# Kernel tuning notes

Hardware: AMD Instinct MI355X
Metric: run time of the kernel (lower is better)

The kernel has to match this reference:

```python
import jax, jax.numpy as jnp
import numpy as np

N, R, IN_DIM, OUT_DIM, MODE = 16, 128, 64, 64, 16


def setup_inputs() -> dict:
    key = jax.random.key(0)
    k1, k2, k3, k4, k5 = jax.random.split(key, 5)
    # xavier_normal-like scale used by the torch init:
    # std = gain * sqrt(2/(fan_in+fan_out)) with gain = sqrt(in+out)/(in*out)
    fan = IN_DIM * OUT_DIM * MODE * MODE  # torch fans over last-dim slices; scale is tiny either way
    w_std = (1.0 / (IN_DIM * OUT_DIM)) * np.sqrt(IN_DIM + OUT_DIM)
    return {
        "X": jax.random.normal(k1, (N, R, R, IN_DIM), dtype=jnp.float32),
        "w_res": jax.random.normal(k2, (IN_DIM, OUT_DIM), dtype=jnp.float32) / np.sqrt(IN_DIM),
        "b_res": jax.random.normal(k3, (OUT_DIM,), dtype=jnp.float32) * 0.01,
        "fw0": jax.random.normal(k4, (IN_DIM, OUT_DIM, MODE, MODE, 2), dtype=jnp.float32) * w_std,
        "fw1": jax.random.normal(k5, (IN_DIM, OUT_DIM, MODE, MODE, 2), dtype=jnp.float32) * w_std,
    }


def reference(X, w_res, b_res, fw0, fw1):
    # X: [N, r, r, in_dim]
    n, r, _, _ = X.shape
    m = MODE
    res = X @ w_res + b_res                          # [N, r, r, out]
    Xp = jnp.transpose(X, (0, 3, 1, 2))              # [N, in, r, r]
    X_ft = jnp.fft.rfft2(Xp, s=(r, r), norm="ortho")  # [N, in, r, r//2+1] complex
    W0 = fw0[..., 0] + 1j * fw0[..., 1]              # [in, out, m, m] complex
    W1 = fw1[..., 0] + 1j * fw1[..., 1]
    top = jnp.einsum("nihw,iohw->nohw", X_ft[:, :, :m, :m], W0)
    bot = jnp.einsum("nihw,iohw->nohw", X_ft[:, :, -m:, :m], W1)
    Out_ft = jnp.zeros((n, OUT_DIM, r, r // 2 + 1), dtype=top.dtype)
    Out_ft = Out_ft.at[:, :, :m, :m].set(top)
    Out_ft = Out_ft.at[:, :, -m:, :m].set(bot)
    Y = jnp.fft.irfft2(Out_ft, s=(r, r), norm="ortho")  # [N, out, r, r]
    Y = jnp.transpose(Y, (0, 2, 3, 1))                   # [N, r, r, out]
    return jax.nn.silu(Y + res)
```

## Files before the change

### kernel.cpp

```cpp
#include <hip/hip_runtime.h>

#define NBATCH 16
#define RSZ 128
#define ICH 64
#define OCH 64
#define MODES 16
#define TMODES 32
#define PI2F 6.283185307179586f

typedef float f32x4 __attribute__((ext_vector_type(4)));
typedef short bf16x8 __attribute__((ext_vector_type(8)));

static __device__ __forceinline__ ushort f2bf(float f) {
  union { float f; unsigned u; } v;
  v.f = f;
  unsigned r = v.u + 0x7FFFu + ((v.u >> 16) & 1u);
  return (ushort)(r >> 16);
}
static __device__ __forceinline__ float b2f(ushort u) {
  union { unsigned u; float f; } v;
  v.u = ((unsigned)u) << 16;
  return v.f;
}

#define TAB_TM 0
#define TAB_EF 4096
#define TAB_WR 8192
#define TAB_T1 12288
#define TAB_E2 28672

__global__ __launch_bounds__(256) void k_prep(const float* __restrict__ fw0,
                                              const float* __restrict__ fw1,
                                              const float* __restrict__ w_res,
                                              ushort* __restrict__ fwT,
                                              ushort* __restrict__ tabs) {
  const int b = blockIdx.x;
  const int tid = threadIdx.x;
  if (b < 128) {
    const int tensor = b >> 6, i = b & 63;
    const float* fw = tensor ? fw1 : fw0;
    const int o = tid & 63, q = tid >> 6;
    const float2* src = (const float2*)fw + ((size_t)(i * 64 + o) * 256 + q * 64);
    ushort2* dst = (ushort2*)fwT;
#pragma unroll 4
    for (int r = 0; r < 64; ++r) {
      float2 v = src[r];
      int mh = q * 4 + (r >> 4), w = r & 15;
      int t = tensor * 16 + mh;
      ushort2 pk;
      pk.x = f2bf(v.x);
      pk.y = f2bf(v.y);
      dst[(((size_t)w * 32 + t) * 64 + i) * 64 + o] = pk;
    }
    return;
  }
  __shared__ float2 ut[128];
  if (tid < 128) {
    float s, c;
    sincosf(PI2F * (float)tid * (1.0f / 128.0f), &s, &c);
    ut[tid] = make_float2(c, s);
  }
  __syncthreads();
  if (b == 128) {
    for (int e = tid; e < 4096; e += 256) {
      int m = e >> 7, x = e & 127, w = m >> 1, c = m & 1;
      float2 u = ut[(w * x) & 127];
      tabs[TAB_TM + e] = f2bf(c ? -u.y : u.x);
    }
  } else if (b == 129) {
    for (int e = tid; e < 4096; e += 256) {
      int x = e >> 5, mm = e & 31, w = mm >> 1, c = mm & 1;
      float2 u = ut[(w * x) & 127];
      tabs[TAB_EF + e] = f2bf(c ? -u.y : u.x);
    }
  } else if (b == 130) {
    for (int e = tid; e < 4096; e += 256) {
      int o = e >> 6, i = e & 63;
      tabs[TAB_WR + e] = f2bf(w_res[i * 64 + o]);
    }
  } else if (b < 135) {
    for (int k = tid; k < 4096; k += 256) {
      int e = (b - 131) * 4096 + k;
      int m = e >> 8, kk = e & 255;
      int y = kk & 127, pl = kk >> 7;
      int t = m & 31, imr = m >> 5;
      int h = (t < 16) ? t : (t + 96);
      float2 u = ut[(h * y) & 127];
      float val = (!imr) ? (pl ? u.y : u.x) : (pl ? u.x : -u.y);
      tabs[TAB_T1 + e] = f2bf(val);
    }
  } else {
    for (int k = tid; k < 4096; k += 256) {
      int e = (b - 135) * 4096 + k;
      int m = e >> 6, kk = e & 63;
      int y = m & 127, imr = m >> 7;
      int t = kk & 31, pl = kk >> 5;
      int h = (t < 16) ? t : (t + 96);
      float2 u = ut[(h * y) & 127];
      float val = (!imr) ? (pl ? -u.y : u.x) : (pl ? u.x : u.y);
      tabs[TAB_E2 + e] = f2bf(val);
    }
  }
}

__global__ __launch_bounds__(256) void k_dftx(const float* __restrict__ X,
                                              const ushort* __restrict__ tabs,
                                              ushort* __restrict__ Are,
                                              ushort* __restrict__ Aim) {
  __shared__ ushort Tm[32][136];
  __shared__ ushort XT[4][64][136];
  const int tid = threadIdx.x;
  const int row0 = blockIdx.x * 4;
  {
    int m = tid >> 3, seg = (tid & 7) * 16;
    *(bf16x8*)&Tm[m][seg] = *(const bf16x8*)&tabs[TAB_TM + m * 128 + seg];
    *(bf16x8*)&Tm[m][seg + 8] = *(const bf16x8*)&tabs[TAB_TM + m * 128 + seg + 8];
  }
  {
    const int rr = tid >> 6, lane = tid & 63;
    const float* Xr = X + (size_t)(row0 + rr) * RSZ * ICH;
    for (int j = 0; j < 8; ++j) {
      int t = lane + 64 * j;
      int i0 = (t & 15) * 4, x0 = (t >> 4) * 4;
      float4 r0 = *(const float4*)&Xr[(x0 + 0) * ICH + i0];
      float4 r1 = *(const float4*)&Xr[(x0 + 1) * ICH + i0];
      float4 r2 = *(const float4*)&Xr[(x0 + 2) * ICH + i0];
      float4 r3 = *(const float4*)&Xr[(x0 + 3) * ICH + i0];
#pragma unroll
      for (int p = 0; p < 4; ++p) {
        int i = i0 + p;
        int col = x0 ^ ((((i) >> 2) & 7) << 3);
        ushort4 pk;
        pk.x = f2bf(((const float*)&r0)[p]);
        pk.y = f2bf(((const float*)&r1)[p]);
        pk.z = f2bf(((const float*)&r2)[p]);
        pk.w = f2bf(((const float*)&r3)[p]);
        *(ushort4*)&XT[rr][i][col] = pk;
      }
    }
  }
  __syncthreads();
  const int wid = tid >> 6, lane = tid & 63;
  const int lr = lane & 15, lk = lane >> 4;
  f32x4 acc[2][4];
#pragma unroll
  for (int mt = 0; mt < 2; ++mt)
#pragma unroll
    for (int nt = 0; nt < 4; ++nt) acc[mt][nt] = (f32x4)(0.f);
#pragma unroll
  for (int kt = 0; kt < 4; ++kt) {
    int kb = kt * 32 + lk * 8;
    bf16x8 a0 = *(const bf16x8*)&Tm[lr][kb];
    bf16x8 a1 = *(const bf16x8*)&Tm[16 + lr][kb];
    bf16x8 b[4];
#pragma unroll
    for (int nt = 0; nt < 4; ++nt) {
      int i = nt * 16 + lr;
      int col = kb ^ (((i >> 2) & 7) << 3);
      b[nt] = *(const bf16x8*)&XT[wid][i][col];
    }
#pragma unroll
    for (int nt = 0; nt < 4; ++nt) {
      acc[0][nt] = __builtin_amdgcn_mfma_f32_16x16x32_bf16(a0, b[nt], acc[0][nt], 0, 0, 0);
      acc[1][nt] = __builtin_amdgcn_mfma_f32_16x16x32_bf16(a1, b[nt], acc[1][nt], 0, 0, 0);
    }
  }
  const int row = row0 + wid;
#pragma unroll
  for (int mt = 0; mt < 2; ++mt)
#pragma unroll
    for (int q = 0; q < 4; ++q) {
      int m = mt * 16 + lk * 4 + q;
      int w = m >> 1, c = m & 1;
      ushort* plane = c ? Aim : Are;
#pragma unroll
      for (int nt = 0; nt < 4; ++nt) {
        int i = nt * 16 + lr;
        plane[((size_t)row * MODES + w) * ICH + i] = f2bf(acc[mt][nt][q]);
      }
    }
}

__global__ __launch_bounds__(512) void k_dfty(const ushort* __restrict__ Are,
                                              const ushort* __restrict__ Aim,
                                              const ushort* __restrict__ tabs,
                                              ushort* __restrict__ B) {
  const int n = blockIdx.x >> 4;
  const int w = blockIdx.x & 15;
  __shared__ ushort T1[64][264];
  __shared__ ushort As[64][264];
  const int tid = threadIdx.x;
  {
    int m = tid >> 3, seg = (tid & 7) * 32;
#pragma unroll
    for (int e = 0; e < 4; ++e)
      *(bf16x8*)&T1[m][seg + e * 8] = *(const bf16x8*)&tabs[TAB_T1 + m * 256 + seg + e * 8];
  }
#pragma unroll
  for (int e = 0; e < 2; ++e) {
    int tt = e * 512 + tid;
    int pl = tt >> 9, r = tt & 511;
    int i0 = (r & 15) * 4, y0 = (r >> 4) * 4;
    const ushort* P = pl ? Aim : Are;
    const ushort* base = P + (((size_t)(n * RSZ + y0) * MODES + w) * ICH + i0);
    ushort4 r0 = *(const ushort4*)(base + 0 * MODES * ICH);
    ushort4 r1 = *(const ushort4*)(base + 1 * MODES * ICH);
    ushort4 r2 = *(const ushort4*)(base + 2 * MODES * ICH);
    ushort4 r3 = *(const ushort4*)(base + 3 * MODES * ICH);
    const ushort* q0 = (const ushort*)&r0;
    const ushort* q1 = (const ushort*)&r1;
    const ushort* q2 = (const ushort*)&r2;
    const ushort* q3 = (const ushort*)&r3;
#pragma unroll
    for (int p = 0; p < 4; ++p) {
      ushort4 pk;
      pk.x = q0[p]; pk.y = q1[p]; pk.z = q2[p]; pk.w = q3[p];
      *(ushort4*)&As[i0 + p][pl * 128 + y0] = pk;
    }
  }
  __syncthreads();
  const int wid = tid >> 6, lane = tid & 63;
  const int lr = lane & 15, lk = lane >> 4;
  const int mt = wid >> 1, nh = wid & 1;
  f32x4 acc[2];
  acc[0] = (f32x4)(0.f);
  acc[1] = (f32x4)(0.f);
#pragma unroll
  for (int kt = 0; kt < 8; ++kt) {
    int kb = kt * 32 + lk * 8;
    bf16x8 a = *(const bf16x8*)&T1[mt * 16 + lr][kb];
    bf16x8 b0 = *(const bf16x8*)&As[(nh * 2 + 0) * 16 + lr][kb];
    bf16x8 b1 = *(const bf16x8*)&As[(nh * 2 + 1) * 16 + lr][kb];
    acc[0] = __builtin_amdgcn_mfma_f32_16x16x32_bf16(a, b0, acc[0], 0, 0, 0);
    acc[1] = __builtin_amdgcn_mfma_f32_16x16x32_bf16(a, b1, acc[1], 0, 0, 0);
  }
#pragma unroll
  for (int nt2 = 0; nt2 < 2; ++nt2)
#pragma unroll
    for (int q = 0; q < 4; ++q) {
      int m = mt * 16 + lk * 4 + q;
      int t = m & 31, pl = m >> 5;
      int i = (nh * 2 + nt2) * 16 + lr;
      B[(((size_t)n * TMODES + t) * MODES + w) * 128 + i * 2 + pl] = f2bf(acc[nt2][q]);
    }
}

__global__ __launch_bounds__(256) void k_mix(ushort* __restrict__ BC,
                                             const ushort* __restrict__ fwT) {
  const int t = blockIdx.x >> 4;
  const int w = blockIdx.x & 15;
  __shared__ float2 bs[NBATCH * ICH];
  __shared__ float2 wsld[ICH * OCH];
  const int tid = threadIdx.x;
  for (int k = tid; k < NBATCH * ICH; k += 256) {
    int n = k >> 6, i = k & 63;
    ushort2 v = *(const ushort2*)&BC[(((size_t)n * TMODES + t) * MODES + w) * 128 + i * 2];
    bs[k] = make_float2(b2f(v.x), b2f(v.y));
  }
  {
    const ushort* Wsl = fwT + ((size_t)(w * 32 + t)) * 8192;
    for (int k4 = tid; k4 < 1024; k4 += 256) {
      bf16x8 v = *(const bf16x8*)(Wsl + k4 * 8);
#pragma unroll
      for (int e = 0; e < 4; ++e)
        wsld[k4 * 4 + e] = make_float2(b2f((ushort)v[2 * e]), b2f((ushort)v[2 * e + 1]));
    }
  }
  __syncthreads();
  const int o = tid & 63;
  const int ng = tid >> 6;
  float2 acc[4] = {{0.f,0.f},{0.f,0.f},{0.f,0.f},{0.f,0.f}};
  for (int i = 0; i < ICH; ++i) {
    float2 wv = wsld[i * OCH + o];
#pragma unroll
    for (int q = 0; q < 4; ++q) {
      float2 bv = bs[(ng * 4 + q) * ICH + i];
      acc[q].x += bv.x * wv.x - bv.y * wv.y;
      acc[q].y += bv.x * wv.y + bv.y * wv.x;
    }
  }
#pragma unroll
  for (int q = 0; q < 4; ++q) {
    int n = ng * 4 + q;
    ushort2 pk;
    pk.x = f2bf(acc[q].x);
    pk.y = f2bf(acc[q].y);
    *(ushort2*)&BC[(((size_t)n * TMODES + t) * MODES + w) * 128 + o * 2] = pk;
  }
}

__global__ __launch_bounds__(512) void k_idfty(const ushort* __restrict__ C,
                                               const ushort* __restrict__ tabs,
                                               ushort* __restrict__ D) {
  const int n = blockIdx.x >> 4;
  const int w = blockIdx.x & 15;
  __shared__ ushort E2[256][72];
  __shared__ ushort Cs[64][72];
  const int tid = threadIdx.x;
  {
    int m = tid >> 1, seg = (tid & 1) * 32;
#pragma unroll
    for (int e = 0; e < 4; ++e)
      *(bf16x8*)&E2[m][seg + e * 8] = *(const bf16x8*)&tabs[TAB_E2 + m * 64 + seg + e * 8];
  }
  const float sc = (w == 0) ? (1.f / 16384.f) : (2.f / 16384.f);
#pragma unroll
  for (int e = 0; e < 4; ++e) {
    int idx = e * 512 + tid;
    int o = idx & 63, t = idx >> 6;
    ushort2 v = *(const ushort2*)&C[(((size_t)n * TMODES + t) * MODES + w) * 128 + o * 2];
    Cs[o][t] = f2bf(b2f(v.x) * sc);
    Cs[o][t + 32] = f2bf(b2f(v.y) * sc);
  }
  __syncthreads();
  const int wid = tid >> 6, lane = tid & 63;
  const int lr = lane & 15, lk = lane >> 4;
  f32x4 acc[2][4];
#pragma unroll
  for (int mi = 0; mi < 2; ++mi)
#pragma unroll
    for (int nt = 0; nt < 4; ++nt) acc[mi][nt] = (f32x4)(0.f);
#pragma unroll
  for (int kt = 0; kt < 2; ++kt) {
    int kb = kt * 32 + lk * 8;
    bf16x8 b[4];
#pragma unroll
    for (int nt = 0; nt < 4; ++nt) b[nt] = *(const bf16x8*)&Cs[nt * 16 + lr][kb];
#pragma unroll
    for (int mi = 0; mi < 2; ++mi) {
      bf16x8 a = *(const bf16x8*)&E2[(wid * 2 + mi) * 16 + lr][kb];
#pragma unroll
      for (int nt = 0; nt < 4; ++nt)
        acc[mi][nt] = __builtin_amdgcn_mfma_f32_16x16x32_bf16(a, b[nt], acc[mi][nt], 0, 0, 0);
    }
  }
#pragma unroll
  for (int mi = 0; mi < 2; ++mi)
#pragma unroll
    for (int nt = 0; nt < 4; ++nt)
#pragma unroll
      for (int q = 0; q < 4; ++q) {
        int m = (wid * 2 + mi) * 16 + lk * 4 + q;
        int y = m & 127, pl = m >> 7;
        int o = nt * 16 + lr;
        D[((size_t)(n * RSZ + y) * MODES + w) * 128 + o * 2 + pl] = f2bf(acc[mi][nt][q]);
      }
}

__global__ __launch_bounds__(256) void k_final(const float* __restrict__ X,
                                               const ushort* __restrict__ D,
                                               const ushort* __restrict__ tabs,
                                               const float* __restrict__ b_res,
                                               float* __restrict__ out) {
  __shared__ ushort Ac[128][104];
  __shared__ ushort Bc[64][104];
  __shared__ float br[64];
  const int tid = threadIdx.x;
  const int row = blockIdx.x;
  const float* Xr = X + (size_t)row * RSZ * ICH;
#pragma unroll
  for (int j = 0; j < 8; ++j) {
    int k = tid + j * 256;
    int x = k >> 4, i0 = (k & 15) * 4;
    float4 v = *(const float4*)&Xr[x * ICH + i0];
    ushort4 pk;
    pk.x = f2bf(v.x); pk.y = f2bf(v.y); pk.z = f2bf(v.z); pk.w = f2bf(v.w);
    *(ushort4*)&Ac[x][i0] = pk;
  }
  {
    int x = tid >> 1, half = tid & 1;
    *(bf16x8*)&Ac[x][64 + half * 16] = *(const bf16x8*)&tabs[TAB_EF + x * 32 + half * 16];
    *(bf16x8*)&Ac[x][64 + half * 16 + 8] = *(const bf16x8*)&tabs[TAB_EF + x * 32 + half * 16 + 8];
  }
  {
    int o = tid >> 2, s = (tid & 3) * 16;
    *(bf16x8*)&Bc[o][s] = *(const bf16x8*)&tabs[TAB_WR + o * 64 + s];
    *(bf16x8*)&Bc[o][s + 8] = *(const bf16x8*)&tabs[TAB_WR + o * 64 + s + 8];
  }
#pragma unroll
  for (int j = 0; j < 4; ++j) {
    int idx = tid + j * 256;
    int w2 = idx >> 6, o = idx & 63;
    ushort2 v = *(const ushort2*)&D[(size_t)row * 2048 + w2 * 128 + o * 2];
    *(ushort2*)&Bc[o][64 + 2 * w2] = v;
  }
  if (tid < 64) br[tid] = b_res[tid];
  __syncthreads();
  const int wid = tid >> 6, lane = tid & 63;
  const int lr = lane & 15, lk = lane >> 4;
  f32x4 acc[2][4];
#pragma unroll
  for (int mi = 0; mi < 2; ++mi)
#pragma unroll
    for (int nt = 0; nt < 4; ++nt) acc[mi][nt] = (f32x4)(0.f);
#pragma unroll
  for (int kt = 0; kt < 3; ++kt) {
    int kb = kt * 32 + lk * 8;
    bf16x8 a0 = *(const bf16x8*)&Ac[(wid * 2 + 0) * 16 + lr][kb];
    bf16x8 a1 = *(const bf16x8*)&Ac[(wid * 2 + 1) * 16 + lr][kb];
    bf16x8 b[4];
#pragma unroll
    for (int nt = 0; nt < 4; ++nt) b[nt] = *(const bf16x8*)&Bc[nt * 16 + lr][kb];
#pragma unroll
    for (int nt = 0; nt < 4; ++nt) {
      acc[0][nt] = __builtin_amdgcn_mfma_f32_16x16x32_bf16(a0, b[nt], acc[0][nt], 0, 0, 0);
      acc[1][nt] = __builtin_amdgcn_mfma_f32_16x16x32_bf16(a1, b[nt], acc[1][nt], 0, 0, 0);
    }
  }
  float* orow = out + (size_t)row * RSZ * OCH;
#pragma unroll
  for (int mi = 0; mi < 2; ++mi)
#pragma unroll
    for (int nt = 0; nt < 4; ++nt)
#pragma unroll
      for (int q = 0; q < 4; ++q) {
        int x = (wid * 2 + mi) * 16 + lk * 4 + q;
        int o = nt * 16 + lr;
        float v = acc[mi][nt][q] + br[o];
        orow[x * OCH + o] = v / (1.f + __expf(-v));
      }
}

extern "C" void kernel_launch(void* const* d_in, const int* in_sizes, int n_in,
                              void* d_out, int out_size, void* d_ws, size_t ws_size,
                              hipStream_t stream) {
  (void)in_sizes; (void)n_in; (void)out_size; (void)ws_size;
  const float* X = (const float*)d_in[0];
  const float* w_res = (const float*)d_in[1];
  const float* b_res = (const float*)d_in[2];
  const float* fw0 = (const float*)d_in[3];
  const float* fw1 = (const float*)d_in[4];
  float* out = (float*)d_out;
  ushort* wsu = (ushort*)d_ws;
  ushort* Are = wsu;
  ushort* Aim = Are + 2097152;
  ushort* Bbf = Aim + 2097152;
  ushort* Dbf = Bbf + 1048576;
  ushort* fwT = Dbf + 4194304;
  ushort* tabs = fwT + 4194304;
  k_prep<<<139, 256, 0, stream>>>(fw0, fw1, w_res, fwT, tabs);
  k_dftx<<<NBATCH * RSZ / 4, 256, 0, stream>>>(X, tabs, Are, Aim);
  k_dfty<<<NBATCH * MODES, 512, 0, stream>>>(Are, Aim, tabs, Bbf);
  k_mix<<<TMODES * MODES, 256, 0, stream>>>(Bbf, fwT);
  k_idfty<<<NBATCH * MODES, 512, 0, stream>>>(Bbf, tabs, Dbf);
  k_final<<<NBATCH * RSZ, 256, 0, stream>>>(X, Dbf, tabs, b_res, out);
}
```

Before: 69.56 us.

## Drop fw transpose pre-pass; cache bf16 X in dftx for final kernel

Removes the 128-block weight transpose/convert pass from k_prep and has k_mix gather the fp32 spectral weights directly from the original layout using strided float2 loads. k_dftx now also writes a bf16 copy of X to workspace, which k_final reads in place of the fp32 X, halving that kernel's input traffic. The trade-offs are uncoalesced 2 KB-strided weight reads in k_mix and an extra 32 MB bf16 write in k_dftx.

```diff
diff --git a/kernel.cpp b/kernel.cpp
--- a/kernel.cpp
+++ b/kernel.cpp
@@ -29,31 +29,10 @@
 #define TAB_T1 12288
 #define TAB_E2 28672
 
-__global__ __launch_bounds__(256) void k_prep(const float* __restrict__ fw0,
-                                              const float* __restrict__ fw1,
-                                              const float* __restrict__ w_res,
-                                              ushort* __restrict__ fwT,
+__global__ __launch_bounds__(256) void k_prep(const float* __restrict__ w_res,
                                               ushort* __restrict__ tabs) {
   const int b = blockIdx.x;
   const int tid = threadIdx.x;
-  if (b < 128) {
-    const int tensor = b >> 6, i = b & 63;
-    const float* fw = tensor ? fw1 : fw0;
-    const int o = tid & 63, q = tid >> 6;
-    const float2* src = (const float2*)fw + ((size_t)(i * 64 + o) * 256 + q * 64);
-    ushort2* dst = (ushort2*)fwT;
-#pragma unroll 4
-    for (int r = 0; r < 64; ++r) {
-      float2 v = src[r];
-      int mh = q * 4 + (r >> 4), w = r & 15;
-      int t = tensor * 16 + mh;
-      ushort2 pk;
-      pk.x = f2bf(v.x);
-      pk.y = f2bf(v.y);
-      dst[(((size_t)w * 32 + t) * 64 + i) * 64 + o] = pk;
-    }
-    return;
-  }
   __shared__ float2 ut[128];
   if (tid < 128) {
     float s, c;
@@ -61,26 +40,26 @@
     ut[tid] = make_float2(c, s);
   }
   __syncthreads();
-  if (b == 128) {
+  if (b == 0) {
     for (int e = tid; e < 4096; e += 256) {
       int m = e >> 7, x = e & 127, w = m >> 1, c = m & 1;
       float2 u = ut[(w * x) & 127];
       tabs[TAB_TM + e] = f2bf(c ? -u.y : u.x);
     }
-  } else if (b == 129) {
+  } else if (b == 1) {
     for (int e = tid; e < 4096; e += 256) {
       int x = e >> 5, mm = e & 31, w = mm >> 1, c = mm & 1;
       float2 u = ut[(w * x) & 127];
       tabs[TAB_EF + e] = f2bf(c ? -u.y : u.x);
     }
-  } else if (b == 130) {
+  } else if (b == 2) {
     for (int e = tid; e < 4096; e += 256) {
       int o = e >> 6, i = e & 63;
       tabs[TAB_WR + e] = f2bf(w_res[i * 64 + o]);
     }
-  } else if (b < 135) {
+  } else if (b < 7) {
     for (int k = tid; k < 4096; k += 256) {
-      int e = (b - 131) * 4096 + k;
+      int e = (b - 3) * 4096 + k;
       int m = e >> 8, kk = e & 255;
       int y = kk & 127, pl = kk >> 7;
       int t = m & 31, imr = m >> 5;
@@ -91,7 +70,7 @@
     }
   } else {
     for (int k = tid; k < 4096; k += 256) {
-      int e = (b - 135) * 4096 + k;
+      int e = (b - 7) * 4096 + k;
       int m = e >> 6, kk = e & 63;
       int y = m & 127, imr = m >> 7;
       int t = kk & 31, pl = kk >> 5;
@@ -106,7 +85,8 @@
 __global__ __launch_bounds__(256) void k_dftx(const float* __restrict__ X,
                                               const ushort* __restrict__ tabs,
                                               ushort* __restrict__ Are,
-                                              ushort* __restrict__ Aim) {
+                                              ushort* __restrict__ Aim,
+                                              ushort* __restrict__ Xbf) {
   __shared__ ushort Tm[32][136];
   __shared__ ushort XT[4][64][136];
   const int tid = threadIdx.x;
@@ -119,6 +99,7 @@
   {
     const int rr = tid >> 6, lane = tid & 63;
     const float* Xr = X + (size_t)(row0 + rr) * RSZ * ICH;
+    ushort* Xbr = Xbf + (size_t)(row0 + rr) * RSZ * ICH;
     for (int j = 0; j < 8; ++j) {
       int t = lane + 64 * j;
       int i0 = (t & 15) * 4, x0 = (t >> 4) * 4;
@@ -126,16 +107,27 @@
       float4 r1 = *(const float4*)&Xr[(x0 + 1) * ICH + i0];
       float4 r2 = *(const float4*)&Xr[(x0 + 2) * ICH + i0];
       float4 r3 = *(const float4*)&Xr[(x0 + 3) * ICH + i0];
+      ushort cc[4][4];
+#pragma unroll
+      for (int e = 0; e < 4; ++e) {
+        cc[0][e] = f2bf(((const float*)&r0)[e]);
+        cc[1][e] = f2bf(((const float*)&r1)[e]);
+        cc[2][e] = f2bf(((const float*)&r2)[e]);
+        cc[3][e] = f2bf(((const float*)&r3)[e]);
+      }
 #pragma unroll
       for (int p = 0; p < 4; ++p) {
         int i = i0 + p;
         int col = x0 ^ ((((i) >> 2) & 7) << 3);
         ushort4 pk;
-        pk.x = f2bf(((const float*)&r0)[p]);
-        pk.y = f2bf(((const float*)&r1)[p]);
-        pk.z = f2bf(((const float*)&r2)[p]);
-        pk.w = f2bf(((const float*)&r3)[p]);
+        pk.x = cc[0][p]; pk.y = cc[1][p]; pk.z = cc[2][p]; pk.w = cc[3][p];
         *(ushort4*)&XT[rr][i][col] = pk;
+      }
+#pragma unroll
+      for (int xr = 0; xr < 4; ++xr) {
+        ushort4 pk;
+        pk.x = cc[xr][0]; pk.y = cc[xr][1]; pk.z = cc[xr][2]; pk.w = cc[xr][3];
+        *(ushort4*)&Xbr[(x0 + xr) * ICH + i0] = pk;
       }
     }
   }
@@ -246,7 +238,8 @@
 }
 
 __global__ __launch_bounds__(256) void k_mix(ushort* __restrict__ BC,
-                                             const ushort* __restrict__ fwT) {
+                                             const float* __restrict__ fw0,
+                                             const float* __restrict__ fw1) {
   const int t = blockIdx.x >> 4;
   const int w = blockIdx.x & 15;
   __shared__ float2 bs[NBATCH * ICH];
@@ -258,12 +251,10 @@
     bs[k] = make_float2(b2f(v.x), b2f(v.y));
   }
   {
-    const ushort* Wsl = fwT + ((size_t)(w * 32 + t)) * 8192;
-    for (int k4 = tid; k4 < 1024; k4 += 256) {
-      bf16x8 v = *(const bf16x8*)(Wsl + k4 * 8);
-#pragma unroll
-      for (int e = 0; e < 4; ++e)
-        wsld[k4 * 4 + e] = make_float2(b2f((ushort)v[2 * e]), b2f((ushort)v[2 * e + 1]));
+    const float* fw = (t < MODES) ? fw0 : fw1;
+    const int mh = t & 15;
+    for (int k = tid; k < ICH * OCH; k += 256) {
+      wsld[k] = *(const float2*)(fw + ((size_t)k * 256 + (size_t)mh * 16 + w) * 2);
     }
   }
   __syncthreads();
@@ -347,7 +338,7 @@
       }
 }
 
-__global__ __launch_bounds__(256) void k_final(const float* __restrict__ X,
+__global__ __launch_bounds__(256) void k_final(const ushort* __restrict__ Xbf,
                                                const ushort* __restrict__ D,
                                                const ushort* __restrict__ tabs,
                                                const float* __restrict__ b_res,
@@ -357,15 +348,12 @@
   __shared__ float br[64];
   const int tid = threadIdx.x;
   const int row = blockIdx.x;
-  const float* Xr = X + (size_t)row * RSZ * ICH;
-#pragma unroll
-  for (int j = 0; j < 8; ++j) {
+  const ushort* Xr = Xbf + (size_t)row * RSZ * ICH;
+#pragma unroll
+  for (int j = 0; j < 4; ++j) {
     int k = tid + j * 256;
-    int x = k >> 4, i0 = (k & 15) * 4;
-    float4 v = *(const float4*)&Xr[x * ICH + i0];
-    ushort4 pk;
-    pk.x = f2bf(v.x); pk.y = f2bf(v.y); pk.z = f2bf(v.z); pk.w = f2bf(v.w);
-    *(ushort4*)&Ac[x][i0] = pk;
+    int x = k >> 3, i0 = (k & 7) * 8;
+    *(bf16x8*)&Ac[x][i0] = *(const bf16x8*)&Xr[x * ICH + i0];
   }
   {
     int x = tid >> 1, half = tid & 1;
@@ -436,12 +424,12 @@
   ushort* Aim = Are + 2097152;
   ushort* Bbf = Aim + 2097152;
   ushort* Dbf = Bbf + 1048576;
-  ushort* fwT = Dbf + 4194304;
-  ushort* tabs = fwT + 4194304;
-  k_prep<<<139, 256, 0, stream>>>(fw0, fw1, w_res, fwT, tabs);
-  k_dftx<<<NBATCH * RSZ / 4, 256, 0, stream>>>(X, tabs, Are, Aim);
+  ushort* Xbf = Dbf + 4194304;
+  ushort* tabs = Xbf + 16777216;
+  k_prep<<<11, 256, 0, stream>>>(w_res, tabs);
+  k_dftx<<<NBATCH * RSZ / 4, 256, 0, stream>>>(X, tabs, Are, Aim, Xbf);
   k_dfty<<<NBATCH * MODES, 512, 0, stream>>>(Are, Aim, tabs, Bbf);
-  k_mix<<<TMODES * MODES, 256, 0, stream>>>(Bbf, fwT);
+  k_mix<<<TMODES * MODES, 256, 0, stream>>>(Bbf, fw0, fw1);
   k_idfty<<<NBATCH * MODES, 512, 0, stream>>>(Bbf, tabs, Dbf);
-  k_final<<<NBATCH * RSZ, 256, 0, stream>>>(X, Dbf, tabs, b_res, out);
-}
+  k_final<<<NBATCH * RSZ, 256, 0, stream>>>(Xbf, Dbf, tabs, b_res, out);
+}
```

Result: slower. 87.39 us (+25.6%).
